# Performance work log

Measured on AMD Instinct MI355X. Metric: run time of the kernel, lower is better.

Reference implementation:

```python
import jax, jax.numpy as jnp
import numpy as np

DIM = 1024
NUM_HEADS = 16
HEAD_DIM = DIM // NUM_HEADS

def setup_inputs() -> dict:
    key = jax.random.key(0)
    ks = jax.random.split(key, 5)
    s = 1.0 / np.sqrt(DIM)
    x = jax.random.normal(ks[0], (2, 2048, DIM), dtype=jnp.float32)
    W_qkv = jax.random.uniform(ks[1], (DIM, 3 * DIM), dtype=jnp.float32, minval=-s, maxval=s)
    b_qkv = jax.random.uniform(ks[2], (3 * DIM,), dtype=jnp.float32, minval=-s, maxval=s)
    W_out = jax.random.uniform(ks[3], (DIM, DIM), dtype=jnp.float32, minval=-s, maxval=s)
    b_out = jax.random.uniform(ks[4], (DIM,), dtype=jnp.float32, minval=-s, maxval=s)
    return {"x": x, "W_qkv": W_qkv, "b_qkv": b_qkv, "W_out": W_out, "b_out": b_out}

def reference(x, W_qkv, b_qkv, W_out, b_out):
    B, S, _ = x.shape
    qkv = x @ W_qkv + b_qkv                       # [B,S,3*dim]
    q, k, v = jnp.split(qkv, 3, axis=-1)
    # [B,S,dim] -> [B,H,S,hd]
    def to_heads(t):
        return t.reshape(B, S, NUM_HEADS, HEAD_DIM).transpose(0, 2, 1, 3)
    q, k, v = to_heads(q), to_heads(k), to_heads(v)
    scale = HEAD_DIM ** -0.5
    scores = jnp.einsum('bhqd,bhkd->bhqk', q, k) * scale
    attn = jax.nn.softmax(scores, axis=-1)
    out = jnp.einsum('bhqk,bhkd->bhqd', attn, v)  # [B,H,S,hd]
    out = out.transpose(0, 2, 1, 3).reshape(B, S, DIM)
    return out @ W_out + b_out
```

## Files before the change

### kernel.cpp

```cpp
#include <hip/hip_runtime.h>
#include <math.h>

#define DIMM    1024
#define NHEADS  16
#define HDIM    64
#define BATCH   2
#define SEQ     2048
#define ROWS    (BATCH*SEQ)

typedef _Float16 f16x8 __attribute__((ext_vector_type(8)));
typedef _Float16 f16x4 __attribute__((ext_vector_type(4)));
typedef float    f32x4 __attribute__((ext_vector_type(4)));

__device__ inline void gl_lds16(const void* g, void* l) {
    __builtin_amdgcn_global_load_lds(
        (const __attribute__((address_space(1))) void*)g,
        (__attribute__((address_space(3))) void*)l, 16, 0, 0);
}

__device__ void tcvt64(const float* __restrict__ in, _Float16* __restrict__ out,
                       int K, int N, int k0, int n0, float (*tile)[65], int t)
{
    {
        const int c4 = (t & 15) * 4;
        const int r  = t >> 4;
        #pragma unroll
        for (int i = 0; i < 4; i++) {
            const int rr = r + 16 * i;
            float4 v = *(const float4*)(in + (size_t)(k0 + rr) * N + n0 + c4);
            tile[rr][c4] = v.x; tile[rr][c4 + 1] = v.y;
            tile[rr][c4 + 2] = v.z; tile[rr][c4 + 3] = v.w;
        }
    }
    __syncthreads();
    #pragma unroll
    for (int i = 0; i < 2; i++) {
        const int seg = t + 256 * i;
        const int n   = seg >> 3;
        const int kc  = (seg & 7) * 8;
        f16x8 o;
        #pragma unroll
        for (int j = 0; j < 8; j++) o[j] = (_Float16)tile[kc + j][n];
        *(f16x8*)(out + (size_t)(n0 + n) * K + k0 + kc) = o;
    }
}

__global__ __launch_bounds__(256)
void prep_kernel(const float* __restrict__ x, const float* __restrict__ Wqkv,
                 const float* __restrict__ Wout, _Float16* __restrict__ xh,
                 _Float16* __restrict__ wqkvt, _Float16* __restrict__ woutt)
{
    __shared__ float tile[64][65];
    const int bx = blockIdx.x;
    const int t  = threadIdx.x;
    if (bx < 2048) {
        const int i = bx * 256 + t;
        const float4 a = *(const float4*)(x + (size_t)i * 8);
        const float4 b = *(const float4*)(x + (size_t)i * 8 + 4);
        f16x8 o;
        o[0] = (_Float16)a.x; o[1] = (_Float16)a.y; o[2] = (_Float16)a.z; o[3] = (_Float16)a.w;
        o[4] = (_Float16)b.x; o[5] = (_Float16)b.y; o[6] = (_Float16)b.z; o[7] = (_Float16)b.w;
        *(f16x8*)(xh + (size_t)i * 8) = o;
    } else if (bx < 2816) {
        const int id = bx - 2048;
        const int gx = id % 48, gy = id / 48;
        tcvt64(Wqkv, wqkvt, DIMM, 3 * DIMM, gy * 64, gx * 64, tile, t);
    } else {
        const int id = bx - 2816;
        const int gx = id & 15, gy = id >> 4;
        tcvt64(Wout, woutt, DIMM, DIMM, gy * 64, gx * 64, tile, t);
    }
}

template<int MODE>
__global__ __launch_bounds__(256)
void hgemm_bias_kernel(const _Float16* __restrict__ A, const _Float16* __restrict__ Bt,
                       const float* __restrict__ bias, void* __restrict__ Cout,
                       _Float16* __restrict__ vtg, int N, int K)
{
    __shared__ _Float16 As[128 * 64];
    __shared__ _Float16 Bs[128 * 64];

    const int t    = threadIdx.x;
    const int w    = t >> 6, lane = t & 63;
    const int quad = lane >> 4, l16 = lane & 15;
    const int wr   = w >> 1, wc = w & 1;
    const int row0 = blockIdx.y * 128, col0 = blockIdx.x * 128;
    const int sw   = l16 & 7;

    f32x4 acc[4][4];
    #pragma unroll
    for (int i = 0; i < 4; i++)
        #pragma unroll
        for (int j = 0; j < 4; j++)
            #pragma unroll
            for (int r = 0; r < 4; r++) acc[i][j][r] = 0.f;

    const _Float16* gA[4];
    const _Float16* gB[4];
    int lofs[4];
    #pragma unroll
    for (int j = 0; j < 4; j++) {
        const int s   = t + 256 * j;
        const int row = s >> 3;
        const int kb  = (s & 7) ^ (row & 7);
        gA[j] = A  + (size_t)(row0 + row) * K + kb * 8;
        gB[j] = Bt + (size_t)(col0 + row) * K + kb * 8;
        lofs[j] = s * 8;
    }

    const int niter = K >> 6;
    #pragma unroll 1
    for (int it = 0; it < niter; it++) {
        __syncthreads();
        #pragma unroll
        for (int j = 0; j < 4; j++) gl_lds16(gA[j], As + lofs[j]);
        #pragma unroll
        for (int j = 0; j < 4; j++) gl_lds16(gB[j], Bs + lofs[j]);
        #pragma unroll
        for (int j = 0; j < 4; j++) { gA[j] += 64; gB[j] += 64; }
        __syncthreads();

        f16x8 af[4][2], bf[4][2];
        #pragma unroll
        for (int i = 0; i < 4; i++) {
            const int arow = wr * 64 + i * 16 + l16;
            const int brow = wc * 64 + i * 16 + l16;
            #pragma unroll
            for (int hh = 0; hh < 2; hh++) {
                af[i][hh] = *(const f16x8*)(As + (arow * 8 + ((hh * 4 + quad) ^ sw)) * 8);
                bf[i][hh] = *(const f16x8*)(Bs + (brow * 8 + ((hh * 4 + quad) ^ sw)) * 8);
            }
        }
        #pragma unroll
        for (int i = 0; i < 4; i++)
            #pragma unroll
            for (int j = 0; j < 4; j++) {
                acc[i][j] = __builtin_amdgcn_mfma_f32_16x16x32_f16(af[i][0], bf[j][0], acc[i][j], 0, 0, 0);
                acc[i][j] = __builtin_amdgcn_mfma_f32_16x16x32_f16(af[i][1], bf[j][1], acc[i][j], 0, 0, 0);
            }
    }

    const bool vblock = (MODE == 1) && (col0 >= 2 * DIMM);
    #pragma unroll
    for (int j = 0; j < 4; j++) {
        const int col = col0 + wc * 64 + j * 16 + l16;
        const float bv = bias[col];
        #pragma unroll
        for (int i = 0; i < 4; i++) {
            const int row = row0 + wr * 64 + i * 16 + quad * 4;
            if (vblock) {
                const int dg  = col - 2 * DIMM;
                const int h   = dg >> 6, dl = dg & 63;
                const int b   = row >> 11, key = row & (SEQ - 1);
                f16x4 o;
                #pragma unroll
                for (int r = 0; r < 4; r++) o[r] = (_Float16)(acc[i][j][r] + bv);
                *(f16x4*)(vtg + ((size_t)((b * NHEADS + h) * 64 + dl)) * SEQ + key) = o;
            } else {
                #pragma unroll
                for (int r = 0; r < 4; r++) {
                    const float v = acc[i][j][r] + bv;
                    if (MODE == 1)
                        ((_Float16*)Cout)[(size_t)(row + r) * N + col] = (_Float16)v;
                    else
                        ((float*)Cout)[(size_t)(row + r) * N + col] = v;
                }
            }
        }
    }
}

__global__ __launch_bounds__(256, 2)
void flash_attn_kernel(const _Float16* __restrict__ qkv,
                       const _Float16* __restrict__ vtg,
                       _Float16* __restrict__ out)
{
    const int qt = blockIdx.x;
    const int bh = blockIdx.y;
    const int b  = bh >> 4, h = bh & 15;
    const int t    = threadIdx.x;
    const int w    = t >> 6;
    const int lane = t & 63;
    const int quad = lane >> 4;
    const int l16  = lane & 15;
    const int sw   = l16 & 7;

    __shared__ __align__(16) _Float16 Ks [64 * 64];
    __shared__ __align__(16) _Float16 Vts[64 * 64];
    __shared__ __align__(16) _Float16 Ps [128 * 72];

    const int q0 = qt * 128;
    const size_t rstr = 3 * DIMM;
    const _Float16* qbase = qkv + (size_t)b * SEQ * rstr;

    f16x8 qf[8][2];
    #pragma unroll
    for (int qb = 0; qb < 8; qb++) {
        const _Float16* qrow = qbase + (size_t)(q0 + qb * 16 + l16) * rstr + h * HDIM;
        qf[qb][0] = *(const f16x8*)(qrow + quad * 8);
        qf[qb][1] = *(const f16x8*)(qrow + 32 + quad * 8);
    }

    f32x4 Oacc[2][4];
    #pragma unroll
    for (int ss = 0; ss < 2; ss++)
        #pragma unroll
        for (int i = 0; i < 4; i++) Oacc[ss][i] = (f32x4){0.f, 0.f, 0.f, 0.f};
    float lrow[8];
    #pragma unroll
    for (int qb = 0; qb < 8; qb++) lrow[qb] = 0.f;

    const int seg0 = t, seg1 = t + 256;
    const int r0 = seg0 >> 3, lb0 = (seg0 & 7) ^ (r0 & 7);
    const int r1 = seg1 >> 3, lb1 = (seg1 & 7) ^ (r1 & 7);
    const _Float16* gK0 = qbase + (size_t)r0 * rstr + DIMM + h * HDIM + lb0 * 8;
    const _Float16* gK1 = qbase + (size_t)r1 * rstr + DIMM + h * HDIM + lb1 * 8;
    const _Float16* gV0 = vtg + ((size_t)bh * 64 + r0) * SEQ + lb0 * 8;
    const _Float16* gV1 = vtg + ((size_t)bh * 64 + r1) * SEQ + lb1 * 8;

    const int kAbase = (16 * w + l16) * 64;

    #pragma unroll 1
    for (int k0 = 0; k0 < SEQ; k0 += 64) {
        __syncthreads();
        gl_lds16(gK0 + (size_t)k0 * rstr, Ks  + seg0 * 8);
        gl_lds16(gK1 + (size_t)k0 * rstr, Ks  + seg1 * 8);
        gl_lds16(gV0 + k0,                Vts + seg0 * 8);
        gl_lds16(gV1 + k0,                Vts + seg1 * 8);
        __syncthreads();

        f16x8 kf0 = *(const f16x8*)(Ks + kAbase + ((0 + quad) ^ sw) * 8);
        f16x8 kf1 = *(const f16x8*)(Ks + kAbase + ((4 + quad) ^ sw) * 8);
        #pragma unroll
        for (int qb = 0; qb < 8; qb++) {
            f32x4 s = (f32x4){0.f, 0.f, 0.f, 0.f};
            s = __builtin_amdgcn_mfma_f32_16x16x32_f16(kf0, qf[qb][0], s, 0, 0, 0);
            s = __builtin_amdgcn_mfma_f32_16x16x32_f16(kf1, qf[qb][1], s, 0, 0, 0);
            float p0 = __expf(s[0] * 0.125f);
            float p1 = __expf(s[1] * 0.125f);
            float p2 = __expf(s[2] * 0.125f);
            float p3 = __expf(s[3] * 0.125f);
            lrow[qb] += (p0 + p1) + (p2 + p3);
            f16x4 pk;
            pk[0] = (_Float16)p0; pk[1] = (_Float16)p1;
            pk[2] = (_Float16)p2; pk[3] = (_Float16)p3;
            *(f16x4*)(Ps + (qb * 16 + l16) * 72 + 16 * w + 4 * quad) = pk;
        }
        __syncthreads();

        f16x8 vf[4][2];
        #pragma unroll
        for (int db = 0; db < 4; db++) {
            const int vrow = db * 16 + l16;
            vf[db][0] = *(const f16x8*)(Vts + vrow * 64 + ((0 + quad) ^ sw) * 8);
            vf[db][1] = *(const f16x8*)(Vts + vrow * 64 + ((4 + quad) ^ sw) * 8);
        }
        #pragma unroll
        for (int ss = 0; ss < 2; ss++) {
            const int prow = ((2 * w + ss) * 16 + l16) * 72;
            f16x8 pf0 = *(const f16x8*)(Ps + prow + quad * 8);
            f16x8 pf1 = *(const f16x8*)(Ps + prow + 32 + quad * 8);
            #pragma unroll
            for (int db = 0; db < 4; db++) {
                Oacc[ss][db] = __builtin_amdgcn_mfma_f32_16x16x32_f16(pf0, vf[db][0], Oacc[ss][db], 0, 0, 0);
                Oacc[ss][db] = __builtin_amdgcn_mfma_f32_16x16x32_f16(pf1, vf[db][1], Oacc[ss][db], 0, 0, 0);
            }
        }
    }

    #pragma unroll
    for (int qb = 0; qb < 8; qb++) {
        lrow[qb] += __shfl_xor(lrow[qb], 16);
        lrow[qb] += __shfl_xor(lrow[qb], 32);
    }
    __syncthreads();
    float* lbuf = (float*)Ks;
    if (lane < 16) {
        #pragma unroll
        for (int qb = 0; qb < 8; qb++) lbuf[w * 128 + qb * 16 + lane] = lrow[qb];
    }
    __syncthreads();
    #pragma unroll
    for (int ss = 0; ss < 2; ss++) {
        const int qloc = 32 * w + ss * 16 + quad * 4;
        float lrec[4];
        #pragma unroll
        for (int r = 0; r < 4; r++) {
            const int q = qloc + r;
            lrec[r] = 1.f / (lbuf[q] + lbuf[128 + q] + lbuf[256 + q] + lbuf[384 + q]);
        }
        #pragma unroll
        for (int db = 0; db < 4; db++) {
            #pragma unroll
            for (int r = 0; r < 4; r++) {
                out[(size_t)(b * SEQ + q0 + qloc + r) * DIMM + h * HDIM + db * 16 + l16] =
                    (_Float16)(Oacc[ss][db][r] * lrec[r]);
            }
        }
    }
}

extern "C" void kernel_launch(void* const* d_in, const int* in_sizes, int n_in,
                              void* d_out, int out_size, void* d_ws, size_t ws_size,
                              hipStream_t stream)
{
    const float* x    = (const float*)d_in[0];
    const float* Wqkv = (const float*)d_in[1];
    const float* bqkv = (const float*)d_in[2];
    const float* Wout = (const float*)d_in[3];
    const float* bout = (const float*)d_in[4];
    float* out = (float*)d_out;

    _Float16* qkvh  = (_Float16*)d_ws;
    _Float16* attnh = qkvh  + (size_t)ROWS * 3 * DIMM;
    _Float16* xh    = attnh + (size_t)ROWS * DIMM;
    _Float16* wqkvt = xh    + (size_t)ROWS * DIMM;
    _Float16* woutt = wqkvt + (size_t)3 * DIMM * DIMM;
    _Float16* vtg   = woutt + (size_t)DIMM * DIMM;

    prep_kernel<<<3072, 256, 0, stream>>>(x, Wqkv, Wout, xh, wqkvt, woutt);
    {
        dim3 grid(3 * DIMM / 128, ROWS / 128);
        hgemm_bias_kernel<1><<<grid, 256, 0, stream>>>(xh, wqkvt, bqkv, qkvh, vtg, 3 * DIMM, DIMM);
    }
    {
        dim3 grid(SEQ / 128, BATCH * NHEADS);
        flash_attn_kernel<<<grid, 256, 0, stream>>>(qkvh, vtg, attnh);
    }
    {
        dim3 grid(DIMM / 128, ROWS / 128);
        hgemm_bias_kernel<0><<<grid, 256, 0, stream>>>(attnh, woutt, bout, out, nullptr, DIMM, DIMM);
    }
}
```

Before: 213.1 us.

## Keep P in registers for PV MFMA, split keys across waves, reduce O in LDS

The attention kernel now feeds the exponentiated scores straight from the QK^T accumulator registers into a 16x16x16 MFMA against V. This removes the Ps shared-memory round trip and the mid-iteration barrier. Each wave covers a 16-key slice and all 64 queries of a 64-query tile, so partial O accumulators are summed across waves through LDS in a serialized epilogue. The query tile is halved to 64, the grid is doubled, occupancy is raised to 3 blocks/SM, and exp uses exp2 with a prescaled log2e constant. In exchange there are more per-block K/V loads and a costly 4-stage reduction epilogue.

```diff
diff --git a/kernel.cpp b/kernel.cpp
--- a/kernel.cpp
+++ b/kernel.cpp
@@ -171,7 +171,7 @@
     }
 }
 
-__global__ __launch_bounds__(256, 2)
+__global__ __launch_bounds__(256, 3)
 void flash_attn_kernel(const _Float16* __restrict__ qkv,
                        const _Float16* __restrict__ vtg,
                        _Float16* __restrict__ out)
@@ -186,30 +186,29 @@
     const int l16  = lane & 15;
     const int sw   = l16 & 7;
 
-    __shared__ __align__(16) _Float16 Ks [64 * 64];
-    __shared__ __align__(16) _Float16 Vts[64 * 64];
-    __shared__ __align__(16) _Float16 Ps [128 * 72];
-
-    const int q0 = qt * 128;
+    __shared__ __align__(16) _Float16 KVs[8192];
+    __shared__ float lbuf[256];
+    _Float16* Ks  = KVs;
+    _Float16* Vts = KVs + 4096;
+
+    const int q0 = qt * 64;
     const size_t rstr = 3 * DIMM;
     const _Float16* qbase = qkv + (size_t)b * SEQ * rstr;
 
-    f16x8 qf[8][2];
-    #pragma unroll
-    for (int qb = 0; qb < 8; qb++) {
+    f16x8 qf[4][2];
+    #pragma unroll
+    for (int qb = 0; qb < 4; qb++) {
         const _Float16* qrow = qbase + (size_t)(q0 + qb * 16 + l16) * rstr + h * HDIM;
         qf[qb][0] = *(const f16x8*)(qrow + quad * 8);
         qf[qb][1] = *(const f16x8*)(qrow + 32 + quad * 8);
     }
 
-    f32x4 Oacc[2][4];
-    #pragma unroll
-    for (int ss = 0; ss < 2; ss++)
-        #pragma unroll
-        for (int i = 0; i < 4; i++) Oacc[ss][i] = (f32x4){0.f, 0.f, 0.f, 0.f};
-    float lrow[8];
-    #pragma unroll
-    for (int qb = 0; qb < 8; qb++) lrow[qb] = 0.f;
+    f32x4 Oacc[4][4];
+    #pragma unroll
+    for (int i = 0; i < 4; i++)
+        #pragma unroll
+        for (int j = 0; j < 4; j++) Oacc[i][j] = (f32x4){0.f, 0.f, 0.f, 0.f};
+    float lrow[4] = {0.f, 0.f, 0.f, 0.f};
 
     const int seg0 = t, seg1 = t + 256;
     const int r0 = seg0 >> 3, lb0 = (seg0 & 7) ^ (r0 & 7);
@@ -220,6 +219,9 @@
     const _Float16* gV1 = vtg + ((size_t)bh * 64 + r1) * SEQ + lb1 * 8;
 
     const int kAbase = (16 * w + l16) * 64;
+    const int vq     = 2 * w + (quad >> 1);
+    const int vsub   = (quad & 1) * 4;
+    const float SCL  = 0.18033688f;
 
     #pragma unroll 1
     for (int k0 = 0; k0 < SEQ; k0 += 64) {
@@ -232,72 +234,98 @@
 
         f16x8 kf0 = *(const f16x8*)(Ks + kAbase + ((0 + quad) ^ sw) * 8);
         f16x8 kf1 = *(const f16x8*)(Ks + kAbase + ((4 + quad) ^ sw) * 8);
-        #pragma unroll
-        for (int qb = 0; qb < 8; qb++) {
+        f16x4 vf[4];
+        #pragma unroll
+        for (int db = 0; db < 4; db++) {
+            const int dl = db * 16 + l16;
+            vf[db] = *(const f16x4*)(Vts + dl * 64 + ((vq ^ sw) << 3) + vsub);
+        }
+
+        #pragma unroll
+        for (int qb = 0; qb < 4; qb++) {
             f32x4 s = (f32x4){0.f, 0.f, 0.f, 0.f};
             s = __builtin_amdgcn_mfma_f32_16x16x32_f16(kf0, qf[qb][0], s, 0, 0, 0);
             s = __builtin_amdgcn_mfma_f32_16x16x32_f16(kf1, qf[qb][1], s, 0, 0, 0);
-            float p0 = __expf(s[0] * 0.125f);
-            float p1 = __expf(s[1] * 0.125f);
-            float p2 = __expf(s[2] * 0.125f);
-            float p3 = __expf(s[3] * 0.125f);
+            float p0 = exp2f(s[0] * SCL);
+            float p1 = exp2f(s[1] * SCL);
+            float p2 = exp2f(s[2] * SCL);
+            float p3 = exp2f(s[3] * SCL);
             lrow[qb] += (p0 + p1) + (p2 + p3);
-            f16x4 pk;
-            pk[0] = (_Float16)p0; pk[1] = (_Float16)p1;
-            pk[2] = (_Float16)p2; pk[3] = (_Float16)p3;
-            *(f16x4*)(Ps + (qb * 16 + l16) * 72 + 16 * w + 4 * quad) = pk;
-        }
-        __syncthreads();
-
-        f16x8 vf[4][2];
-        #pragma unroll
-        for (int db = 0; db < 4; db++) {
-            const int vrow = db * 16 + l16;
-            vf[db][0] = *(const f16x8*)(Vts + vrow * 64 + ((0 + quad) ^ sw) * 8);
-            vf[db][1] = *(const f16x8*)(Vts + vrow * 64 + ((4 + quad) ^ sw) * 8);
-        }
-        #pragma unroll
-        for (int ss = 0; ss < 2; ss++) {
-            const int prow = ((2 * w + ss) * 16 + l16) * 72;
-            f16x8 pf0 = *(const f16x8*)(Ps + prow + quad * 8);
-            f16x8 pf1 = *(const f16x8*)(Ps + prow + 32 + quad * 8);
-            #pragma unroll
-            for (int db = 0; db < 4; db++) {
-                Oacc[ss][db] = __builtin_amdgcn_mfma_f32_16x16x32_f16(pf0, vf[db][0], Oacc[ss][db], 0, 0, 0);
-                Oacc[ss][db] = __builtin_amdgcn_mfma_f32_16x16x32_f16(pf1, vf[db][1], Oacc[ss][db], 0, 0, 0);
-            }
-        }
-    }
-
-    #pragma unroll
-    for (int qb = 0; qb < 8; qb++) {
+            f16x4 pa;
+            pa[0] = (_Float16)p0; pa[1] = (_Float16)p1;
+            pa[2] = (_Float16)p2; pa[3] = (_Float16)p3;
+            #pragma unroll
+            for (int db = 0; db < 4; db++)
+                Oacc[qb][db] = __builtin_amdgcn_mfma_f32_16x16x16f16(pa, vf[db], Oacc[qb][db], 0, 0, 0);
+        }
+    }
+
+    #pragma unroll
+    for (int qb = 0; qb < 4; qb++) {
         lrow[qb] += __shfl_xor(lrow[qb], 16);
         lrow[qb] += __shfl_xor(lrow[qb], 32);
     }
     __syncthreads();
-    float* lbuf = (float*)Ks;
     if (lane < 16) {
         #pragma unroll
-        for (int qb = 0; qb < 8; qb++) lbuf[w * 128 + qb * 16 + lane] = lrow[qb];
-    }
-    __syncthreads();
-    #pragma unroll
-    for (int ss = 0; ss < 2; ss++) {
-        const int qloc = 32 * w + ss * 16 + quad * 4;
-        float lrec[4];
-        #pragma unroll
-        for (int r = 0; r < 4; r++) {
-            const int q = qloc + r;
-            lrec[r] = 1.f / (lbuf[q] + lbuf[128 + q] + lbuf[256 + q] + lbuf[384 + q]);
-        }
-        #pragma unroll
-        for (int db = 0; db < 4; db++) {
-            #pragma unroll
-            for (int r = 0; r < 4; r++) {
-                out[(size_t)(b * SEQ + q0 + qloc + r) * DIMM + h * HDIM + db * 16 + l16] =
-                    (_Float16)(Oacc[ss][db][r] * lrec[r]);
-            }
-        }
+        for (int qb = 0; qb < 4; qb++) lbuf[w * 64 + qb * 16 + lane] = lrow[qb];
+    }
+
+    float* Obuf = (float*)KVs;
+    if (w == 0) {
+        #pragma unroll
+        for (int qb = 0; qb < 4; qb++)
+            #pragma unroll
+            for (int db = 0; db < 4; db++)
+                #pragma unroll
+                for (int r = 0; r < 4; r++)
+                    Obuf[(qb * 16 + quad * 4 + r) * 64 + db * 16 + l16] = Oacc[qb][db][r];
+    }
+    __syncthreads();
+    if (w == 1) {
+        #pragma unroll
+        for (int qb = 0; qb < 4; qb++)
+            #pragma unroll
+            for (int db = 0; db < 4; db++)
+                #pragma unroll
+                for (int r = 0; r < 4; r++)
+                    Obuf[(qb * 16 + quad * 4 + r) * 64 + db * 16 + l16] += Oacc[qb][db][r];
+    }
+    __syncthreads();
+    if (w == 2) {
+        #pragma unroll
+        for (int qb = 0; qb < 4; qb++)
+            #pragma unroll
+            for (int db = 0; db < 4; db++)
+                #pragma unroll
+                for (int r = 0; r < 4; r++)
+                    Obuf[(qb * 16 + quad * 4 + r) * 64 + db * 16 + l16] += Oacc[qb][db][r];
+    }
+    __syncthreads();
+    if (w == 3) {
+        #pragma unroll
+        for (int qb = 0; qb < 4; qb++)
+            #pragma unroll
+            for (int db = 0; db < 4; db++)
+                #pragma unroll
+                for (int r = 0; r < 4; r++)
+                    Obuf[(qb * 16 + quad * 4 + r) * 64 + db * 16 + l16] += Oacc[qb][db][r];
+    }
+    __syncthreads();
+
+    {
+        const int row = t >> 2, d0 = (t & 3) * 16;
+        const float lr = 1.f / (lbuf[row] + lbuf[64 + row] + lbuf[128 + row] + lbuf[192 + row]);
+        const float* ob = Obuf + row * 64 + d0;
+        f16x8 o0, o1;
+        #pragma unroll
+        for (int j = 0; j < 8; j++) {
+            o0[j] = (_Float16)(ob[j] * lr);
+            o1[j] = (_Float16)(ob[8 + j] * lr);
+        }
+        _Float16* orow = out + (size_t)(b * SEQ + q0 + row) * DIMM + h * HDIM + d0;
+        *(f16x8*)orow       = o0;
+        *(f16x8*)(orow + 8) = o1;
     }
 }
 
@@ -325,7 +353,7 @@
         hgemm_bias_kernel<1><<<grid, 256, 0, stream>>>(xh, wqkvt, bqkv, qkvh, vtg, 3 * DIMM, DIMM);
     }
     {
-        dim3 grid(SEQ / 128, BATCH * NHEADS);
+        dim3 grid(SEQ / 64, BATCH * NHEADS);
         flash_attn_kernel<<<grid, 256, 0, stream>>>(qkvh, vtg, attnh);
     }
     {
```

Result: slower. 225.7 us (+5.9%).
